# Kernel tuning notes

Measured on AMD Instinct MI355X. Metric: run time of the kernel, lower is better.

Reference implementation:

```python
import jax, jax.numpy as jnp
import numpy as np

EPS = 1e-5  # BatchNorm eps (torch default)


def gcn_conv(x, W, b, src, dst, ew, n_nodes):
    """PyG GCNConv with normalize=True, add_self_loops=True (fill_value=1.0).
    Self-loop contribution handled analytically instead of appending edges."""
    xw = x @ W  # [N, out]
    # degree including self-loop weight 1.0 (PyG sums weights at the target node)
    deg = jax.ops.segment_sum(ew, dst, num_segments=n_nodes) + 1.0  # [N]
    dinv = jnp.where(deg > 0, jax.lax.rsqrt(deg), 0.0)
    norm = dinv[src] * ew * dinv[dst]  # [E]
    agg = jax.ops.segment_sum(xw[src] * norm[:, None], dst, num_segments=n_nodes)
    agg = agg + xw * (dinv * dinv)[:, None]  # self-loop message
    return agg + b


def batch_norm(x, gamma, beta):
    m = jnp.mean(x, axis=0)
    v = jnp.var(x, axis=0)  # biased, matches torch BN normalization
    return gamma * (x - m) * jax.lax.rsqrt(v + EPS) + beta


def setup_inputs() -> dict:
    key = jax.random.key(0)
    ks = jax.random.split(key, 12)
    N, E, D_IN, D_H, D_OUT = 100000, 1600000, 128, 128, 40
    x = jax.random.normal(ks[0], (N, D_IN), dtype=jnp.float32)
    edge_index = jax.random.randint(ks[1], (2, E), 0, N, dtype=jnp.int64)
    edge_weight = jax.random.uniform(ks[2], (E,), dtype=jnp.float32)
    def lin(k, fi, fo):
        s = 1.0 / np.sqrt(fi)
        return jax.random.uniform(k, (fi, fo), dtype=jnp.float32, minval=-s, maxval=s)
    return {
        "x": x, "edge_index": edge_index, "edge_weight": edge_weight,
        "W0": lin(ks[3], D_IN, D_H), "b0": jnp.zeros((D_H,), jnp.float32),
        "g0": jnp.ones((D_H,), jnp.float32), "be0": jnp.zeros((D_H,), jnp.float32),
        "W1": lin(ks[4], D_H, D_H), "b1": jnp.zeros((D_H,), jnp.float32),
        "g1": jnp.ones((D_H,), jnp.float32), "be1": jnp.zeros((D_H,), jnp.float32),
        "W2": lin(ks[5], D_H, D_OUT), "b2": jnp.zeros((D_OUT,), jnp.float32),
    }


def reference(x, edge_index, edge_weight, W0, b0, g0, be0, W1, b1, g1, be1, W2, b2):
    n_nodes = x.shape[0]
    src, dst = edge_index[0], edge_index[1]
    # layer 0: GCNConv -> BN -> ReLU (dropout identity: deterministic/eval)
    h = gcn_conv(x, W0, b0, src, dst, edge_weight, n_nodes)
    h = jax.nn.relu(batch_norm(h, g0, be0))
    # layer 1
    h = gcn_conv(h, W1, b1, src, dst, edge_weight, n_nodes)
    h = jax.nn.relu(batch_norm(h, g1, be1))
    # last conv + log_softmax over classes
    h = gcn_conv(h, W2, b2, src, dst, edge_weight, n_nodes)
    return jax.nn.log_softmax(h, axis=-1)
```

## Files before the change

kernel.cpp:

```cpp
#include <hip/hip_runtime.h>
#include <math.h>


#define CHUNK 8192

__device__ __forceinline__ float2 bf2_unpack(unsigned u) {
    float2 r;
    r.x = __uint_as_float(u << 16);
    r.y = __uint_as_float(u & 0xffff0000u);
    return r;
}
__device__ __forceinline__ unsigned bf2_pack(float a, float b) {
    unsigned ua = __float_as_uint(a);
    unsigned ub = __float_as_uint(b);
    ua = (ua + 0x7fffu + ((ua >> 16) & 1u)) >> 16;
    ub = (ub + 0x7fffu + ((ub >> 16) & 1u)) >> 16;
    return ua | (ub << 16);
}

__global__ void k_detect(const unsigned* __restrict__ raw, int nsample, int* __restrict__ flag) {
    int i = blockIdx.x * blockDim.x + threadIdx.x;
    if (i < nsample) {
        if (raw[2 * i + 1] != 0u) atomicOr(flag, 1);
    }
}

__device__ __forceinline__ int edge_src(const unsigned* raw, int e, int E, int is64) {
    return is64 ? (int)raw[2 * (size_t)e] : (int)raw[e];
}
__device__ __forceinline__ int edge_dst(const unsigned* raw, int e, int E, int is64) {
    return is64 ? (int)raw[2 * ((size_t)E + e)] : (int)raw[(size_t)E + e];
}

__global__ __launch_bounds__(256) void k_bhist(const unsigned* __restrict__ raw,
                                               int* __restrict__ bhist, int* __restrict__ chist,
                                               const int* __restrict__ flag,
                                               int E, int NB, int nchunks) {
    __shared__ int h[512];
    int is64 = (*flag == 0);
    for (int c = blockIdx.x; c < nchunks; c += gridDim.x) {
        for (int t = threadIdx.x; t < 512; t += 256) h[t] = 0;
        __syncthreads();
        int base = c * CHUNK;
        int end = (base + CHUNK < E) ? base + CHUNK : E;
        for (int e = base + threadIdx.x; e < end; e += 256) {
            int d = edge_dst(raw, e, E, is64);
            atomicAdd(&h[d >> 8], 1);
        }
        __syncthreads();
        for (int t = threadIdx.x; t < NB; t += 256) {
            int v = h[t];
            chist[(size_t)c * 512 + t] = v;
            if (v) atomicAdd(&bhist[t], v);
        }
        __syncthreads();
    }
}

__global__ __launch_bounds__(512) void k_bscan(const int* __restrict__ bhist,
                                               int* __restrict__ bstart,
                                               int* __restrict__ bcur, int NB) {
    __shared__ int s[512];
    int tid = threadIdx.x;
    int v = (tid < NB) ? bhist[tid] : 0;
    s[tid] = v;
    __syncthreads();
    for (int off = 1; off < 512; off <<= 1) {
        int t = (tid >= off) ? s[tid - off] : 0;
        __syncthreads();
        if (tid >= off) s[tid] += t;
        __syncthreads();
    }
    int ex = s[tid] - v;
    if (tid <= NB) {
        int val = (tid < NB) ? ex : s[NB > 0 ? NB - 1 : 0];
        bstart[tid] = val;
        if (tid < NB) bcur[tid] = val;
    }
}

__global__ __launch_bounds__(256) void k_part(const unsigned* __restrict__ raw,
                                              const float* __restrict__ ew,
                                              const int* __restrict__ chist,
                                              int* __restrict__ bcur, int2* __restrict__ staging,
                                              const int* __restrict__ flag,
                                              int E, int NB, int nchunks) {
    __shared__ int cur[512];
    int is64 = (*flag == 0);
    for (int c = blockIdx.x; c < nchunks; c += gridDim.x) {
        for (int t = threadIdx.x; t < NB; t += 256) {
            int v = chist[(size_t)c * 512 + t];
            cur[t] = v ? atomicAdd(&bcur[t], v) : 0;
        }
        __syncthreads();
        int base = c * CHUNK;
        int end = (base + CHUNK < E) ? base + CHUNK : E;
        for (int e = base + threadIdx.x; e < end; e += 256) {
            int s = edge_src(raw, e, E, is64);
            int d = edge_dst(raw, e, E, is64);
            float w = ew[e];
            int pos = atomicAdd(&cur[d >> 8], 1);
            staging[pos] = make_int2(s | ((d & 255) << 24), __float_as_int(w));
        }
        __syncthreads();
    }
}

__global__ __launch_bounds__(256) void k_bucket(const int* __restrict__ bstart,
                                                const int2* __restrict__ staging,
                                                int* __restrict__ rowptr, float* __restrict__ dinv,
                                                int2* __restrict__ ep, int N, int NB) {
    __shared__ int cnt[256];
    __shared__ float dw[256];
    __shared__ int sc[256];
    __shared__ int cur[256];

    const int b = blockIdx.x;
    const int t = threadIdx.x;
    const int n0 = b << 8;
    const int nn = (N - n0 < 256) ? (N - n0) : 256;
    const int es = bstart[b], ee = bstart[b + 1];

    cnt[t] = 0;
    dw[t] = 0.f;
    __syncthreads();

    for (int j = es + t; j < ee; j += 256) {
        int2 p = staging[j];
        int dl = ((unsigned)p.x) >> 24;
        atomicAdd(&cnt[dl], 1);
        atomicAdd(&dw[dl], __int_as_float(p.y));
    }
    __syncthreads();

    int v = cnt[t];
    sc[t] = v;
    __syncthreads();
    for (int off = 1; off < 256; off <<= 1) {
        int tv = (t >= off) ? sc[t - off] : 0;
        __syncthreads();
        if (t >= off) sc[t] += tv;
        __syncthreads();
    }
    int exoff = sc[t] - v;
    cur[t] = es + exoff;
    if (t < nn) {
        rowptr[n0 + t] = es + exoff;
        dinv[n0 + t] = rsqrtf(dw[t] + 1.0f);
    }
    if (t == 0) rowptr[(n0 + 256 < N) ? (n0 + 256) : N] = ee;
    __syncthreads();

    for (int j = es + t; j < ee; j += 256) {
        int2 p = staging[j];
        int dl = ((unsigned)p.x) >> 24;
        int pos = atomicAdd(&cur[dl], 1);
        ep[pos] = make_int2(p.x & 0x00ffffff, p.y);
    }
}

template <int DOUT, int KC, bool BN>
__global__ __launch_bounds__(256) void k_gemm(
    const float* __restrict__ X, const unsigned* __restrict__ Xp,
    const float* __restrict__ W,
    const float* __restrict__ scale, const float* __restrict__ shift,
    const float* __restrict__ dscale, unsigned* __restrict__ Y, int N)
{
    constexpr int NCH = 128 / KC;
    constexpr int NDW = DOUT / 2;
    __shared__ __align__(16) float Wl[KC * DOUT];
    __shared__ __align__(16) float Xs[4][8 * 128];
    __shared__ float sc_l[128], sh_l[128];

    const int tid = threadIdx.x;
    const int wave = tid >> 6, lane = tid & 63;
    if (BN) {
        if (tid < 128) { sc_l[tid] = scale[tid]; sh_l[tid] = shift[tid]; }
    }
    __syncthreads();

    const int srow = lane >> 3;
    const int skk = (lane & 7) * 16;

    for (int base = blockIdx.x * 32; base < N; base += gridDim.x * 32) {
        {
            int r = base + wave * 8 + srow;
            float vf[16];
            if (BN) {
                uint4 u0 = make_uint4(0, 0, 0, 0), u1 = u0;
                if (r < N) {
                    const uint4* p = (const uint4*)(Xp + (size_t)r * 64 + (lane & 7) * 8);
                    u0 = p[0]; u1 = p[1];
                }
                unsigned uu[8] = {u0.x, u0.y, u0.z, u0.w, u1.x, u1.y, u1.z, u1.w};
#pragma unroll
                for (int d = 0; d < 8; d++) {
                    float2 f = bf2_unpack(uu[d]);
                    vf[2 * d] = f.x;
                    vf[2 * d + 1] = f.y;
                }
#pragma unroll
                for (int j = 0; j < 16; j++)
                    vf[j] = fmaxf(vf[j] * sc_l[skk + j] + sh_l[skk + j], 0.f);
            } else {
                float4 v[4];
                if (r < N) {
                    const float4* p = (const float4*)(X + (size_t)r * 128 + skk);
                    v[0] = p[0]; v[1] = p[1]; v[2] = p[2]; v[3] = p[3];
                } else {
                    v[0] = v[1] = v[2] = v[3] = make_float4(0.f, 0.f, 0.f, 0.f);
                }
#pragma unroll
                for (int j = 0; j < 16; j++) vf[j] = ((const float*)v)[j];
            }
            float4* q = (float4*)&Xs[wave][srow * 128 + skk];
#pragma unroll
            for (int d = 0; d < 4; d++)
                q[d] = make_float4(vf[4 * d], vf[4 * d + 1], vf[4 * d + 2], vf[4 * d + 3]);
        }

        float acc0[8], acc1[8];
#pragma unroll
        for (int r = 0; r < 8; r++) { acc0[r] = 0.f; acc1[r] = 0.f; }

        for (int ch = 0; ch < NCH; ++ch) {
            __syncthreads();
            for (int idx = tid; idx < KC * DOUT / 4; idx += 256)
                ((float4*)Wl)[idx] = ((const float4*)(W + (size_t)ch * KC * DOUT))[idx];
            __syncthreads();

            for (int k = 0; k < KC; k += 4) {
                float4 a[8];
#pragma unroll
                for (int r = 0; r < 8; r++)
                    a[r] = *(const float4*)&Xs[wave][r * 128 + ch * KC + k];
#pragma unroll
                for (int kk = 0; kk < 4; kk++) {
                    float2 wv = make_float2(0.f, 0.f);
                    if (lane < NDW)
                        wv = *(const float2*)&Wl[(k + kk) * DOUT + 2 * lane];
#pragma unroll
                    for (int r = 0; r < 8; r++) {
                        float av = ((const float*)&a[r])[kk];
                        acc0[r] += av * wv.x;
                        acc1[r] += av * wv.y;
                    }
                }
            }
        }

#pragma unroll
        for (int r = 0; r < 8; r++) {
            int row = base + wave * 8 + r;
            if (row < N && lane < NDW) {
                float rs = dscale[row];
                Y[(size_t)row * NDW + lane] = bf2_pack(acc0[r] * rs, acc1[r] * rs);
            }
        }
    }
}

__global__ __launch_bounds__(256) void k_agg128(
    const unsigned* __restrict__ xw, const int* __restrict__ rowptr,
    const unsigned long long* __restrict__ ep, const float* __restrict__ dinv,
    const float* __restrict__ bias, unsigned* __restrict__ h,
    float* __restrict__ bn_sum, float* __restrict__ bn_sq, int N)
{
    __shared__ float redS[512], redQ[512];
    const int lane = threadIdx.x & 63;
    const int wave = threadIdx.x >> 6;
    const int base = blockIdx.x * 64 + wave * 16;
    const float b0 = bias[2 * lane], b1 = bias[2 * lane + 1];
    float s0 = 0.f, s1 = 0.f, q0 = 0.f, q1 = 0.f;

    const int nmax = (N - base < 16) ? (N - base) : 16;
    for (int n = 0; n < nmax; n++) {
        const int i = base + n;
        const int rs = rowptr[i], re = rowptr[i + 1];
        const float di = dinv[i];
        float2 sv = bf2_unpack(xw[(size_t)i * 64 + lane]);
        float acc0 = sv.x, acc1 = sv.y;
        int j = rs;
        for (; j + 8 <= re; j += 8) {
            unsigned long long u0 = __builtin_nontemporal_load(ep + j);
            unsigned long long u1 = __builtin_nontemporal_load(ep + j + 1);
            unsigned long long u2 = __builtin_nontemporal_load(ep + j + 2);
            unsigned long long u3 = __builtin_nontemporal_load(ep + j + 3);
            unsigned long long u4 = __builtin_nontemporal_load(ep + j + 4);
            unsigned long long u5 = __builtin_nontemporal_load(ep + j + 5);
            unsigned long long u6 = __builtin_nontemporal_load(ep + j + 6);
            unsigned long long u7 = __builtin_nontemporal_load(ep + j + 7);
            unsigned v0 = xw[(size_t)(unsigned)u0 * 64 + lane];
            unsigned v1 = xw[(size_t)(unsigned)u1 * 64 + lane];
            unsigned v2 = xw[(size_t)(unsigned)u2 * 64 + lane];
            unsigned v3 = xw[(size_t)(unsigned)u3 * 64 + lane];
            unsigned v4 = xw[(size_t)(unsigned)u4 * 64 + lane];
            unsigned v5 = xw[(size_t)(unsigned)u5 * 64 + lane];
            unsigned v6 = xw[(size_t)(unsigned)u6 * 64 + lane];
            unsigned v7 = xw[(size_t)(unsigned)u7 * 64 + lane];
            float c0 = __int_as_float((int)(u0 >> 32)), c1 = __int_as_float((int)(u1 >> 32));
            float c2 = __int_as_float((int)(u2 >> 32)), c3 = __int_as_float((int)(u3 >> 32));
            float c4 = __int_as_float((int)(u4 >> 32)), c5 = __int_as_float((int)(u5 >> 32));
            float c6 = __int_as_float((int)(u6 >> 32)), c7 = __int_as_float((int)(u7 >> 32));
            float2 f0 = bf2_unpack(v0), f1 = bf2_unpack(v1);
            float2 f2 = bf2_unpack(v2), f3 = bf2_unpack(v3);
            float2 f4 = bf2_unpack(v4), f5 = bf2_unpack(v5);
            float2 f6 = bf2_unpack(v6), f7 = bf2_unpack(v7);
            acc0 += c0 * f0.x + c1 * f1.x + c2 * f2.x + c3 * f3.x
                  + c4 * f4.x + c5 * f5.x + c6 * f6.x + c7 * f7.x;
            acc1 += c0 * f0.y + c1 * f1.y + c2 * f2.y + c3 * f3.y
                  + c4 * f4.y + c5 * f5.y + c6 * f6.y + c7 * f7.y;
        }
        for (; j + 4 <= re; j += 4) {
            unsigned long long u0 = __builtin_nontemporal_load(ep + j);
            unsigned long long u1 = __builtin_nontemporal_load(ep + j + 1);
            unsigned long long u2 = __builtin_nontemporal_load(ep + j + 2);
            unsigned long long u3 = __builtin_nontemporal_load(ep + j + 3);
            unsigned v0 = xw[(size_t)(unsigned)u0 * 64 + lane];
            unsigned v1 = xw[(size_t)(unsigned)u1 * 64 + lane];
            unsigned v2 = xw[(size_t)(unsigned)u2 * 64 + lane];
            unsigned v3 = xw[(size_t)(unsigned)u3 * 64 + lane];
            float c0 = __int_as_float((int)(u0 >> 32)), c1 = __int_as_float((int)(u1 >> 32));
            float c2 = __int_as_float((int)(u2 >> 32)), c3 = __int_as_float((int)(u3 >> 32));
            float2 f0 = bf2_unpack(v0), f1 = bf2_unpack(v1);
            float2 f2 = bf2_unpack(v2), f3 = bf2_unpack(v3);
            acc0 += c0 * f0.x + c1 * f1.x + c2 * f2.x + c3 * f3.x;
            acc1 += c0 * f0.y + c1 * f1.y + c2 * f2.y + c3 * f3.y;
        }
        for (; j < re; j++) {
            unsigned long long u = __builtin_nontemporal_load(ep + j);
            float c = __int_as_float((int)(u >> 32));
            float2 f = bf2_unpack(xw[(size_t)(unsigned)u * 64 + lane]);
            acc0 += c * f.x;
            acc1 += c * f.y;
        }
        acc0 = acc0 * di + b0;
        acc1 = acc1 * di + b1;
        __builtin_nontemporal_store(bf2_pack(acc0, acc1), &h[(size_t)i * 64 + lane]);
        s0 += acc0; s1 += acc1; q0 += acc0 * acc0; q1 += acc1 * acc1;
    }

    redS[wave * 128 + 2 * lane] = s0;
    redS[wave * 128 + 2 * lane + 1] = s1;
    redQ[wave * 128 + 2 * lane] = q0;
    redQ[wave * 128 + 2 * lane + 1] = q1;
    __syncthreads();
    if (threadIdx.x < 128) {
        int f = threadIdx.x;
        float ts = redS[f] + redS[128 + f] + redS[256 + f] + redS[384 + f];
        float tq = redQ[f] + redQ[128 + f] + redQ[256 + f] + redQ[384 + f];
        atomicAdd(&bn_sum[f], ts);
        atomicAdd(&bn_sq[f], tq);
    }
}

__global__ void k_bnfin(const float* __restrict__ bn_sum, const float* __restrict__ bn_sq,
                        const float* __restrict__ gamma, const float* __restrict__ beta,
                        float* __restrict__ scale, float* __restrict__ shift, int N) {
    int f = threadIdx.x;
    float inv = 1.0f / (float)N;
    float m = bn_sum[f] * inv;
    float v = bn_sq[f] * inv - m * m;
    float sc = gamma[f] * rsqrtf(v + 1e-5f);
    scale[f] = sc;
    shift[f] = beta[f] - m * sc;
}

__global__ __launch_bounds__(256) void k_agg40(
    const unsigned* __restrict__ xw, const int* __restrict__ rowptr,
    const unsigned long long* __restrict__ ep, const float* __restrict__ dinv,
    const float* __restrict__ bias, float* __restrict__ out, int N)
{
    const int lane = threadIdx.x & 63;
    const int wave = threadIdx.x >> 6;
    const int half = lane >> 5;
    const int col = lane & 31;
    const bool act = col < 20;
    const int base = blockIdx.x * 64 + wave * 16;
    if (base >= N) return;
    const int cc = act ? col : 0;
    const float b0 = act ? bias[2 * col] : 0.f;
    const float b1 = act ? bias[2 * col + 1] : 0.f;

    for (int n = 0; n < 16; n += 2) {
        const int i = base + n + half;
        const bool valid = i < N;
        const int ic = valid ? i : 0;
        const int rs = rowptr[ic];
        int re = rowptr[ic + 1];
        re = valid ? re : rs;
        const float di = dinv[ic];
        float2 sv = bf2_unpack(xw[(size_t)ic * 20 + cc]);
        float acc0 = sv.x, acc1 = sv.y;
        int j = rs;
        for (; j + 8 <= re; j += 8) {
            unsigned long long u0 = __builtin_nontemporal_load(ep + j);
            unsigned long long u1 = __builtin_nontemporal_load(ep + j + 1);
            unsigned long long u2 = __builtin_nontemporal_load(ep + j + 2);
            unsigned long long u3 = __builtin_nontemporal_load(ep + j + 3);
            unsigned long long u4 = __builtin_nontemporal_load(ep + j + 4);
            unsigned long long u5 = __builtin_nontemporal_load(ep + j + 5);
            unsigned long long u6 = __builtin_nontemporal_load(ep + j + 6);
            unsigned long long u7 = __builtin_nontemporal_load(ep + j + 7);
            unsigned v0 = xw[(size_t)(unsigned)u0 * 20 + cc];
            unsigned v1 = xw[(size_t)(unsigned)u1 * 20 + cc];
            unsigned v2 = xw[(size_t)(unsigned)u2 * 20 + cc];
            unsigned v3 = xw[(size_t)(unsigned)u3 * 20 + cc];
            unsigned v4 = xw[(size_t)(unsigned)u4 * 20 + cc];
            unsigned v5 = xw[(size_t)(unsigned)u5 * 20 + cc];
            unsigned v6 = xw[(size_t)(unsigned)u6 * 20 + cc];
            unsigned v7 = xw[(size_t)(unsigned)u7 * 20 + cc];
            float c0 = __int_as_float((int)(u0 >> 32)), c1 = __int_as_float((int)(u1 >> 32));
            float c2 = __int_as_float((int)(u2 >> 32)), c3 = __int_as_float((int)(u3 >> 32));
            float c4 = __int_as_float((int)(u4 >> 32)), c5 = __int_as_float((int)(u5 >> 32));
            float c6 = __int_as_float((int)(u6 >> 32)), c7 = __int_as_float((int)(u7 >> 32));
            float2 f0 = bf2_unpack(v0), f1 = bf2_unpack(v1);
            float2 f2 = bf2_unpack(v2), f3 = bf2_unpack(v3);
            float2 f4 = bf2_unpack(v4), f5 = bf2_unpack(v5);
            float2 f6 = bf2_unpack(v6), f7 = bf2_unpack(v7);
            acc0 += c0 * f0.x + c1 * f1.x + c2 * f2.x + c3 * f3.x
                  + c4 * f4.x + c5 * f5.x + c6 * f6.x + c7 * f7.x;
            acc1 += c0 * f0.y + c1 * f1.y + c2 * f2.y + c3 * f3.y
                  + c4 * f4.y + c5 * f5.y + c6 * f6.y + c7 * f7.y;
        }
        for (; j < re; j++) {
            unsigned long long u = __builtin_nontemporal_load(ep + j);
            float c = __int_as_float((int)(u >> 32));
            float2 f = bf2_unpack(xw[(size_t)(unsigned)u * 20 + cc]);
            acc0 += c * f.x;
            acc1 += c * f.y;
        }
        acc0 = acc0 * di + b0;
        acc1 = acc1 * di + b1;

        float m = act ? fmaxf(acc0, acc1) : -1e30f;
#pragma unroll
        for (int off = 16; off; off >>= 1) m = fmaxf(m, __shfl_xor(m, off));
        float ex = act ? (expf(acc0 - m) + expf(acc1 - m)) : 0.f;
#pragma unroll
        for (int off = 16; off; off >>= 1) ex += __shfl_xor(ex, off);
        float ls = logf(ex);
        if (act && valid)
            *(float2*)&out[(size_t)i * 40 + 2 * col] = make_float2(acc0 - m - ls, acc1 - m - ls);
    }
}

extern "C" void kernel_launch(void* const* d_in, const int* in_sizes, int n_in,
                              void* d_out, int out_size, void* d_ws, size_t ws_size,
                              hipStream_t stream) {
    const float* x   = (const float*)d_in[0];
    const unsigned* ei = (const unsigned*)d_in[1];
    const float* ew  = (const float*)d_in[2];
    const float* W0  = (const float*)d_in[3];
    const float* b0  = (const float*)d_in[4];
    const float* g0  = (const float*)d_in[5];
    const float* be0 = (const float*)d_in[6];
    const float* W1  = (const float*)d_in[7];
    const float* b1  = (const float*)d_in[8];
    const float* g1  = (const float*)d_in[9];
    const float* be1 = (const float*)d_in[10];
    const float* W2  = (const float*)d_in[11];
    const float* b2  = (const float*)d_in[12];

    const int N = in_sizes[0] / 128;
    const int E = in_sizes[2];
    if (N <= 0 || E <= 0) return;
    const int NB = (N + 255) >> 8;
    const int nchunks = (E + CHUNK - 1) / CHUNK;

    char* ws = (char*)d_ws;
    size_t off = 0;
    auto carve = [&](size_t bytes) {
        char* p = ws + off;
        off += (bytes + 511) & ~((size_t)511);
        return p;
    };
    unsigned* F       = (unsigned*)carve((size_t)N * 64 * 4);
    unsigned* P       = (unsigned*)carve((size_t)N * 64 * 4);
    int2*     ep      = (int2*)carve((size_t)E * 8);
    int2*     staging = (int2*)carve((size_t)E * 8);
    int*      chist   = (int*)carve((size_t)nchunks * 512 * 4);
    int*      rowptr  = (int*)carve((size_t)(N + 1) * 4);
    float*    dinv    = (float*)carve((size_t)N * 4);
    int*      bhist   = (int*)carve(513 * 4);
    int*      bstart  = (int*)carve(513 * 4);
    int*      bcur    = (int*)carve(513 * 4);
    float*    bn      = (float*)carve(512 * 4);
    int*      flag    = (int*)carve(64);

    hipMemsetAsync(bhist, 0, 513 * 4, stream);
    hipMemsetAsync(flag, 0, 4, stream);

    int nsample = E < 4096 ? E : 4096;
    k_detect<<<(nsample + 255) / 256, 256, 0, stream>>>(ei, nsample, flag);
    int pgrid = nchunks < 1024 ? nchunks : 1024;
    k_bhist<<<pgrid, 256, 0, stream>>>(ei, bhist, chist, flag, E, NB, nchunks);
    k_bscan<<<1, 512, 0, stream>>>(bhist, bstart, bcur, NB);
    k_part<<<pgrid, 256, 0, stream>>>(ei, ew, chist, bcur, staging, flag, E, NB, nchunks);
    k_bucket<<<NB, 256, 0, stream>>>(bstart, staging, rowptr, dinv, ep, N, NB);

    const int gemm_grid = 768;
    const int agg_grid = (N + 63) / 64;
    const unsigned long long* epu = (const unsigned long long*)ep;

    k_gemm<128, 64, false><<<gemm_grid, 256, 0, stream>>>(x, nullptr, W0, nullptr, nullptr, dinv, P, N);
    hipMemsetAsync(bn, 0, 1024, stream);
    k_agg128<<<agg_grid, 256, 0, stream>>>(P, rowptr, epu, dinv, b0, F, bn, bn + 128, N);
    k_bnfin<<<1, 128, 0, stream>>>(bn, bn + 128, g0, be0, bn + 256, bn + 384, N);

    k_gemm<128, 64, true><<<gemm_grid, 256, 0, stream>>>(nullptr, F, W1, bn + 256, bn + 384, dinv, P, N);
    hipMemsetAsync(bn, 0, 1024, stream);
    k_agg128<<<agg_grid, 256, 0, stream>>>(P, rowptr, epu, dinv, b1, F, bn, bn + 128, N);
    k_bnfin<<<1, 128, 0, stream>>>(bn, bn + 128, g1, be1, bn + 256, bn + 384, N);

    k_gemm<40, 128, true><<<gemm_grid, 256, 0, stream>>>(nullptr, F, W2, bn + 256, bn + 384, dinv, P, N);
    k_agg40<<<agg_grid, 256, 0, stream>>>(P, rowptr, epu, dinv, b2, (float*)d_out, N);
}
```

Before: 665.5 us.

## Replace scalar FP32 GEMMs with bf16 MFMA kernels and shrink aggregation blocks

Replaces the three FP32 FMA-loop GEMMs with a matrix-core kernel that converts inputs and weights to bf16 in LDS and uses 32x32x16 bf16 MFMA instructions, with the BN+ReLU and degree scaling fused into the load and store. The aggregation kernels also move from 64 to 32 nodes per block, giving more blocks for better load balance. The GEMM inputs for the first layer now round to bf16, which adds precision loss, and the weight transpose into LDS is redone in every block.

```diff
diff --git a/kernel.cpp b/kernel.cpp
--- a/kernel.cpp
+++ b/kernel.cpp
@@ -3,6 +3,9 @@
 
 
 #define CHUNK 8192
+
+typedef __attribute__((ext_vector_type(8))) short short8v;
+typedef __attribute__((ext_vector_type(16))) float float16v;
 
 __device__ __forceinline__ float2 bf2_unpack(unsigned u) {
     float2 r;
@@ -16,6 +19,19 @@
     ua = (ua + 0x7fffu + ((ua >> 16) & 1u)) >> 16;
     ub = (ub + 0x7fffu + ((ub >> 16) & 1u)) >> 16;
     return ua | (ub << 16);
+}
+__device__ __forceinline__ short bf16r(float x) {
+    unsigned u = __float_as_uint(x);
+    u = (u + 0x7fffu + ((u >> 16) & 1u)) >> 16;
+    return (short)u;
+}
+__device__ __forceinline__ short8v lds_read8(const short* p) {
+    short4 lo = *(const short4*)p;
+    short4 hi = *(const short4*)(p + 4);
+    short8v r;
+    r[0] = lo.x; r[1] = lo.y; r[2] = lo.z; r[3] = lo.w;
+    r[4] = hi.x; r[5] = hi.y; r[6] = hi.z; r[7] = hi.w;
+    return r;
 }
 
 __global__ void k_detect(const unsigned* __restrict__ raw, int nsample, int* __restrict__ flag) {
@@ -159,102 +175,104 @@
     }
 }
 
-template <int DOUT, int KC, bool BN>
-__global__ __launch_bounds__(256) void k_gemm(
-    const float* __restrict__ X, const unsigned* __restrict__ Xp,
-    const float* __restrict__ W,
-    const float* __restrict__ scale, const float* __restrict__ shift,
-    const float* __restrict__ dscale, unsigned* __restrict__ Y, int N)
+template <int DOUT, int NCT, bool BN, bool FP32IN>
+__global__ __launch_bounds__(256) void k_gemm_mfma(
+    const float* __restrict__ Xf, const unsigned* __restrict__ Xp,
+    const float* __restrict__ W, const float* __restrict__ scale,
+    const float* __restrict__ shift, const float* __restrict__ dscale,
+    unsigned* __restrict__ Y, int N)
 {
-    constexpr int NCH = 128 / KC;
     constexpr int NDW = DOUT / 2;
-    __shared__ __align__(16) float Wl[KC * DOUT];
-    __shared__ __align__(16) float Xs[4][8 * 128];
-    __shared__ float sc_l[128], sh_l[128];
+    constexpr int LDK = 132;
+    constexpr int WROWS = (NCT == 4) ? 128 : 64;
+    constexpr int RTPW = (NCT == 4) ? 2 : 1;
+    __shared__ short Wt[WROWS][LDK];
+    __shared__ short As[64][LDK];
+    __shared__ float scL[128], shL[128], dscL[64];
 
     const int tid = threadIdx.x;
-    const int wave = tid >> 6, lane = tid & 63;
-    if (BN) {
-        if (tid < 128) { sc_l[tid] = scale[tid]; sh_l[tid] = shift[tid]; }
-    }
-    __syncthreads();
-
-    const int srow = lane >> 3;
-    const int skk = (lane & 7) * 16;
-
-    for (int base = blockIdx.x * 32; base < N; base += gridDim.x * 32) {
-        {
-            int r = base + wave * 8 + srow;
-            float vf[16];
-            if (BN) {
-                uint4 u0 = make_uint4(0, 0, 0, 0), u1 = u0;
-                if (r < N) {
-                    const uint4* p = (const uint4*)(Xp + (size_t)r * 64 + (lane & 7) * 8);
-                    u0 = p[0]; u1 = p[1];
+    const int wv = tid >> 6, ln = tid & 63;
+    const int m = ln & 31, q = ln >> 5;
+    const int ct = wv % NCT;
+    const int rtbase = (NCT == 4) ? 0 : (wv >> 1);
+
+    if (BN && tid < 128) { scL[tid] = scale[tid]; shL[tid] = shift[tid]; }
+    for (int i = tid; i < WROWS * 128; i += 256) {
+        int n = i % WROWS, k = i / WROWS;
+        float w = (n < DOUT) ? W[k * DOUT + n] : 0.f;
+        Wt[n][k] = bf16r(w);
+    }
+
+    for (int base = blockIdx.x * 64; base < N; base += gridDim.x * 64) {
+        __syncthreads();
+        if (FP32IN) {
+            for (int i = tid; i < 64 * 32; i += 256) {
+                int r = i >> 5, s = i & 31;
+                int row = base + r;
+                float4 v = make_float4(0.f, 0.f, 0.f, 0.f);
+                if (row < N) v = ((const float4*)(Xf + (size_t)row * 128))[s];
+                short4 qv = make_short4(bf16r(v.x), bf16r(v.y), bf16r(v.z), bf16r(v.w));
+                *(short4*)&As[r][s * 4] = qv;
+            }
+        } else {
+            for (int i = tid; i < 64 * 16; i += 256) {
+                int r = i >> 4, s = i & 15;
+                int row = base + r;
+                uint4 u = make_uint4(0, 0, 0, 0);
+                if (row < N) u = ((const uint4*)(Xp + (size_t)row * 64))[s];
+                unsigned uu[4] = {u.x, u.y, u.z, u.w};
+                short vv[8];
+#pragma unroll
+                for (int d = 0; d < 4; d++) {
+                    float2 f = bf2_unpack(uu[d]);
+                    int fi = s * 8 + 2 * d;
+                    f.x = fmaxf(f.x * scL[fi] + shL[fi], 0.f);
+                    f.y = fmaxf(f.y * scL[fi + 1] + shL[fi + 1], 0.f);
+                    vv[2 * d] = bf16r(f.x);
+                    vv[2 * d + 1] = bf16r(f.y);
                 }
-                unsigned uu[8] = {u0.x, u0.y, u0.z, u0.w, u1.x, u1.y, u1.z, u1.w};
-#pragma unroll
-                for (int d = 0; d < 8; d++) {
-                    float2 f = bf2_unpack(uu[d]);
-                    vf[2 * d] = f.x;
-                    vf[2 * d + 1] = f.y;
+                *(short4*)&As[r][s * 8] = make_short4(vv[0], vv[1], vv[2], vv[3]);
+                *(short4*)&As[r][s * 8 + 4] = make_short4(vv[4], vv[5], vv[6], vv[7]);
+            }
+        }
+        if (tid < 64) {
+            int row = base + tid;
+            dscL[tid] = (row < N) ? dscale[row] : 0.f;
+        }
+        __syncthreads();
+
+        float16v acc[RTPW];
+#pragma unroll
+        for (int rt = 0; rt < RTPW; rt++)
+#pragma unroll
+            for (int r = 0; r < 16; r++) acc[rt][r] = 0.f;
+
+#pragma unroll
+        for (int kc = 0; kc < 8; kc++) {
+            int kb = kc * 16 + q * 8;
+            short8v bfrag = lds_read8(&Wt[ct * 32 + m][kb]);
+#pragma unroll
+            for (int rt = 0; rt < RTPW; rt++) {
+                int rtg = (NCT == 4) ? rt : rtbase;
+                short8v afrag = lds_read8(&As[rtg * 32 + m][kb]);
+                acc[rt] = __builtin_amdgcn_mfma_f32_32x32x16_bf16(afrag, bfrag, acc[rt], 0, 0, 0);
+            }
+        }
+
+#pragma unroll
+        for (int rt = 0; rt < RTPW; rt++) {
+            int rtg = (NCT == 4) ? rt : rtbase;
+#pragma unroll
+            for (int r = 0; r < 16; r++) {
+                int rowl = rtg * 32 + (r & 3) + 8 * (r >> 2) + 4 * q;
+                float v = acc[rt][r] * dscL[rowl];
+                float pv = __shfl_xor(v, 1);
+                if (!(ln & 1)) {
+                    int row = base + rowl;
+                    int cp = ct * 16 + (m >> 1);
+                    if (row < N && cp < NDW)
+                        __builtin_nontemporal_store(bf2_pack(v, pv), &Y[(size_t)row * NDW + cp]);
                 }
-#pragma unroll
-                for (int j = 0; j < 16; j++)
-                    vf[j] = fmaxf(vf[j] * sc_l[skk + j] + sh_l[skk + j], 0.f);
-            } else {
-                float4 v[4];
-                if (r < N) {
-                    const float4* p = (const float4*)(X + (size_t)r * 128 + skk);
-                    v[0] = p[0]; v[1] = p[1]; v[2] = p[2]; v[3] = p[3];
-                } else {
-                    v[0] = v[1] = v[2] = v[3] = make_float4(0.f, 0.f, 0.f, 0.f);
-                }
-#pragma unroll
-                for (int j = 0; j < 16; j++) vf[j] = ((const float*)v)[j];
-            }
-            float4* q = (float4*)&Xs[wave][srow * 128 + skk];
-#pragma unroll
-            for (int d = 0; d < 4; d++)
-                q[d] = make_float4(vf[4 * d], vf[4 * d + 1], vf[4 * d + 2], vf[4 * d + 3]);
-        }
-
-        float acc0[8], acc1[8];
-#pragma unroll
-        for (int r = 0; r < 8; r++) { acc0[r] = 0.f; acc1[r] = 0.f; }
-
-        for (int ch = 0; ch < NCH; ++ch) {
-            __syncthreads();
-            for (int idx = tid; idx < KC * DOUT / 4; idx += 256)
-                ((float4*)Wl)[idx] = ((const float4*)(W + (size_t)ch * KC * DOUT))[idx];
-            __syncthreads();
-
-            for (int k = 0; k < KC; k += 4) {
-                float4 a[8];
-#pragma unroll
-                for (int r = 0; r < 8; r++)
-                    a[r] = *(const float4*)&Xs[wave][r * 128 + ch * KC + k];
-#pragma unroll
-                for (int kk = 0; kk < 4; kk++) {
-                    float2 wv = make_float2(0.f, 0.f);
-                    if (lane < NDW)
-                        wv = *(const float2*)&Wl[(k + kk) * DOUT + 2 * lane];
-#pragma unroll
-                    for (int r = 0; r < 8; r++) {
-                        float av = ((const float*)&a[r])[kk];
-                        acc0[r] += av * wv.x;
-                        acc1[r] += av * wv.y;
-                    }
-                }
-            }
-        }
-
-#pragma unroll
-        for (int r = 0; r < 8; r++) {
-            int row = base + wave * 8 + r;
-            if (row < N && lane < NDW) {
-                float rs = dscale[row];
-                Y[(size_t)row * NDW + lane] = bf2_pack(acc0[r] * rs, acc1[r] * rs);
             }
         }
     }
@@ -269,11 +287,11 @@
     __shared__ float redS[512], redQ[512];
     const int lane = threadIdx.x & 63;
     const int wave = threadIdx.x >> 6;
-    const int base = blockIdx.x * 64 + wave * 16;
+    const int base = blockIdx.x * 32 + wave * 8;
     const float b0 = bias[2 * lane], b1 = bias[2 * lane + 1];
     float s0 = 0.f, s1 = 0.f, q0 = 0.f, q1 = 0.f;
 
-    const int nmax = (N - base < 16) ? (N - base) : 16;
+    const int nmax = (N - base < 8) ? (N - base) : 8;
     for (int n = 0; n < nmax; n++) {
         const int i = base + n;
         const int rs = rowptr[i], re = rowptr[i + 1];
@@ -376,13 +394,13 @@
     const int half = lane >> 5;
     const int col = lane & 31;
     const bool act = col < 20;
-    const int base = blockIdx.x * 64 + wave * 16;
+    const int base = blockIdx.x * 32 + wave * 8;
     if (base >= N) return;
     const int cc = act ? col : 0;
     const float b0 = act ? bias[2 * col] : 0.f;
     const float b1 = act ? bias[2 * col + 1] : 0.f;
 
-    for (int n = 0; n < 16; n += 2) {
+    for (int n = 0; n < 8; n += 2) {
         const int i = base + n + half;
         const bool valid = i < N;
         const int ic = valid ? i : 0;
@@ -499,20 +517,19 @@
     k_part<<<pgrid, 256, 0, stream>>>(ei, ew, chist, bcur, staging, flag, E, NB, nchunks);
     k_bucket<<<NB, 256, 0, stream>>>(bstart, staging, rowptr, dinv, ep, N, NB);
 
-    const int gemm_grid = 768;
-    const int agg_grid = (N + 63) / 64;
+    const int agg_grid = (N + 31) / 32;
     const unsigned long long* epu = (const unsigned long long*)ep;
 
-    k_gemm<128, 64, false><<<gemm_grid, 256, 0, stream>>>(x, nullptr, W0, nullptr, nullptr, dinv, P, N);
+    k_gemm_mfma<128, 4, false, true><<<1024, 256, 0, stream>>>(x, nullptr, W0, nullptr, nullptr, dinv, P, N);
     hipMemsetAsync(bn, 0, 1024, stream);
     k_agg128<<<agg_grid, 256, 0, stream>>>(P, rowptr, epu, dinv, b0, F, bn, bn + 128, N);
     k_bnfin<<<1, 128, 0, stream>>>(bn, bn + 128, g0, be0, bn + 256, bn + 384, N);
 
-    k_gemm<128, 64, true><<<gemm_grid, 256, 0, stream>>>(nullptr, F, W1, bn + 256, bn + 384, dinv, P, N);
+    k_gemm_mfma<128, 4, true, false><<<1024, 256, 0, stream>>>(nullptr, F, W1, bn + 256, bn + 384, dinv, P, N);
     hipMemsetAsync(bn, 0, 1024, stream);
     k_agg128<<<agg_grid, 256, 0, stream>>>(P, rowptr, epu, dinv, b1, F, bn, bn + 128, N);
     k_bnfin<<<1, 128, 0, stream>>>(bn, bn + 128, g1, be1, bn + 256, bn + 384, N);
 
-    k_gemm<40, 128, true><<<gemm_grid, 256, 0, stream>>>(nullptr, F, W2, bn + 256, bn + 384, dinv, P, N);
+    k_gemm_mfma<40, 2, true, false><<<1024, 256, 0, stream>>>(nullptr, F, W2, bn + 256, bn + 384, dinv, P, N);
     k_agg40<<<agg_grid, 256, 0, stream>>>(P, rowptr, epu, dinv, b2, (float*)d_out, N);
 }
```

Result: faster. 586.8 us (-11.8%).
